# Kernel tuning notes

Measured on AMD Instinct MI355X. Metric: run time of the kernel, lower is better.

Reference implementation:

```python
import jax, jax.numpy as jnp
import numpy as np

HID_GNN = 64
HID_LSTM = 128
FUTURE = 24
N_HYDRO = 32
N_METEO = 64
B, T, E = 32, 168, 384
SLOPE = 0.01  # F.leaky_relu default


def setup_inputs() -> dict:
    key = jax.random.key(0)
    ks = jax.random.split(key, 12)
    N = N_HYDRO + N_METEO
    data_meteo = jax.random.normal(ks[0], (B, T, N_METEO, 1), jnp.float32)
    data_hydro = jax.random.normal(ks[1], (B, T, N_HYDRO, 1), jnp.float32)
    edge_index = jax.random.randint(ks[2], (2, E), 0, N, dtype=jnp.int64)
    # GraphConv(1, HID_GNN): out = lin_root(x) + lin_rel(sum_j x_j) + bias
    W_root = jax.random.normal(ks[3], (HID_GNN, 1), jnp.float32) * 1.0
    W_rel = jax.random.normal(ks[4], (HID_GNN, 1), jnp.float32) * 1.0
    b_gnn = jnp.zeros((HID_GNN,), jnp.float32)
    # Per-station LSTM weights (torch gate order i,f,g,o), stacked over stations
    sih = 1.0 / np.sqrt(HID_GNN)
    shh = 1.0 / np.sqrt(HID_LSTM)
    Wih = jax.random.normal(ks[5], (N_HYDRO, 4 * HID_LSTM, HID_GNN), jnp.float32) * sih
    Whh = jax.random.normal(ks[6], (N_HYDRO, 4 * HID_LSTM, HID_LSTM), jnp.float32) * shh
    bih = jnp.zeros((N_HYDRO, 4 * HID_LSTM), jnp.float32)
    bhh = jnp.zeros((N_HYDRO, 4 * HID_LSTM), jnp.float32)
    W_lin = jax.random.normal(ks[7], (FUTURE, HID_LSTM), jnp.float32) * shh
    b_lin = jnp.zeros((FUTURE,), jnp.float32)
    return {"data_meteo": data_meteo, "data_hydro": data_hydro, "edge_index": edge_index,
            "W_root": W_root, "W_rel": W_rel, "b_gnn": b_gnn,
            "Wih": Wih, "Whh": Whh, "bih": bih, "bhh": bhh,
            "W_lin": W_lin, "b_lin": b_lin}


def _lstm_last(xs, Wih_s, Whh_s, b_s):
    # xs: [B,T,D]; one station's LSTM; returns last hidden [B,H]
    H = Whh_s.shape[1]
    h0 = jnp.zeros((xs.shape[0], H), xs.dtype)

    def step(carry, xt):
        h, c = carry
        gates = xt @ Wih_s.T + h @ Whh_s.T + b_s  # [B,4H]
        i, f, g, o = jnp.split(gates, 4, axis=-1)
        c = jax.nn.sigmoid(f) * c + jax.nn.sigmoid(i) * jnp.tanh(g)
        h = jax.nn.sigmoid(o) * jnp.tanh(c)
        return (h, c), None

    (hT, _), _ = jax.lax.scan(step, (h0, h0), jnp.swapaxes(xs, 0, 1))
    return hT


def reference(data_meteo, data_hydro, edge_index, W_root, W_rel, b_gnn,
              Wih, Whh, bih, bhh, W_lin, b_lin):
    Bn, Tn, Nh, F = data_hydro.shape
    Nm = data_meteo.shape[2]
    N = Nh + Nm
    # [B,T,N,1] -> one graph per (b,t); same edge_index in every graph
    x = jnp.concatenate([data_hydro, data_meteo], axis=2).reshape(Bn * Tn, N, F)
    src, dst = edge_index[0], edge_index[1]
    agg = jnp.zeros_like(x).at[:, dst].add(x[:, src])  # sum aggregation
    h = x @ W_root.T + agg @ W_rel.T + b_gnn          # GraphConv, [G,N,HID_GNN]
    h = jax.nn.leaky_relu(h, SLOPE)
    hydro = h.reshape(Bn, Tn, N, -1)[:, :, :Nh, :]    # [B,T,Nh,HID_GNN]
    # per-station LSTM: vmap over station axis with station-specific weights
    last = jax.vmap(_lstm_last, in_axes=(2, 0, 0, 0))(hydro, Wih, Whh, bih + bhh)  # [Nh,B,H]
    pred = last @ W_lin.T + b_lin                     # [Nh,B,FUTURE]
    pred = jnp.swapaxes(pred, 0, 1)                   # [B,Nh,FUTURE]
    return jax.nn.leaky_relu(pred, SLOPE)
```

## Files before the change

kernel.cpp:

```cpp
#include <hip/hip_runtime.h>

typedef unsigned short u16;
typedef unsigned int u32;
typedef __attribute__((ext_vector_type(8))) short short8;
typedef __attribute__((ext_vector_type(4))) float floatx4;
typedef __attribute__((ext_vector_type(4))) float float4v;

#define B_ 32
#define T_ 168
#define NH_ 32
#define NM_ 64
#define E_ 384
#define HL_ 128
#define FUT_ 24
#define SLOPE_ 0.01f
#define XP_ 80
#define HP_ 144
#define WIH_LP 72
#define WHH_LP 136
#define OVL_E (T_ * 4 * XP_)

static __device__ __forceinline__ float b2f(u16 u) {
  u32 v = ((u32)u) << 16;
  return __builtin_bit_cast(float, v);
}
static __device__ __forceinline__ u16 f2bf(float f) {
  u32 x = __builtin_bit_cast(u32, f);
  u32 r = (x + 0x7fffu + ((x >> 16) & 1u)) >> 16;
  return (u16)r;
}
static __device__ __forceinline__ float fexp2(float x) { return __builtin_amdgcn_exp2f(x); }
static __device__ __forceinline__ float frcp(float x) { return __builtin_amdgcn_rcpf(x); }
static __device__ __forceinline__ float sigm(float x) {
  return frcp(1.0f + fexp2(-1.4426950408889634f * x));
}
static __device__ __forceinline__ float tanh_fast(float x) {
  return 1.0f - 2.0f * frcp(1.0f + fexp2(2.8853900817779268f * x));
}
static __device__ __forceinline__ float sel4(floatx4 v, int r) {
  float m0 = (r & 1) ? v[1] : v[0];
  float m1 = (r & 1) ? v[3] : v[2];
  return (r & 2) ? m1 : m0;
}
static __device__ __forceinline__ float lrelu(float x) { return fmaxf(x, SLOPE_ * x); }

__launch_bounds__(512, 2)
__global__ void fused_kernel(const float* __restrict__ dm, const float* __restrict__ dh,
                             const int* __restrict__ eidx,
                             const float* __restrict__ Wroot, const float* __restrict__ Wrel,
                             const float* __restrict__ bgnn,
                             const float* __restrict__ Wih, const float* __restrict__ Whh,
                             const float* __restrict__ bih, const float* __restrict__ bhh,
                             const float* __restrict__ Wlin, const float* __restrict__ blin,
                             float* __restrict__ out) {
  const int s = blockIdx.x & 31;
  const int bg = blockIdx.x >> 5;
  const int tid = threadIdx.x;
  const int w = tid >> 6;
  const int lane = tid & 63;
  const int cm = lane & 15;
  const int q = lane >> 4;
  const int b = cm & 3;
  const int rho = cm >> 2;

  __shared__ __align__(16) u16 ovl[OVL_E];
  __shared__ __align__(16) u16 hbuf[2 * 4 * HP_];
  __shared__ float xh_lds[4][T_];
  __shared__ float ag_lds[4][T_];
  __shared__ float wr_s[64], wv_s[64], bg_s[64];
  __shared__ int srcs[E_];
  __shared__ int nsrc, iflag;

  if (tid == 0) { nsrc = 0; iflag = 0; }
  for (int i = tid; i < 2 * 4 * HP_; i += 512) hbuf[i] = 0;
  __syncthreads();

  {
    int odd = 0;
    for (int e = tid; e < E_; e += 512) odd |= eidx[2 * e + 1];
    if (odd) atomicOr(&iflag, 1);
  }
  __syncthreads();
  const bool i32 = iflag != 0;

  for (int e = tid; e < E_; e += 512) {
    int se = i32 ? eidx[e] : eidx[2 * e];
    int de = i32 ? eidx[E_ + e] : eidx[2 * E_ + 2 * e];
    if (de == s) { int i = atomicAdd(&nsrc, 1); srcs[i] = se; }
  }
  if (tid < 64) { wr_s[tid] = Wroot[tid]; wv_s[tid] = Wrel[tid]; bg_s[tid] = bgnn[tid]; }
  for (int i = tid; i < 4 * T_; i += 512) {
    int bb = i / T_, t = i % T_;
    xh_lds[bb][t] = dh[((size_t)(bg * 4 + bb) * T_ + t) * NH_ + s];
  }
  floatx4 bias_init[4];
#pragma unroll
  for (int blk = 0; blk < 4; blk++)
#pragma unroll
    for (int r = 0; r < 4; r++) {
      const int nb = blk * 128 + w * 16 + q * 4 + r;
      bias_init[blk][r] = bih[s * 512 + nb] + bhh[s * 512 + nb];
    }
  __syncthreads();

  const int ns = nsrc;
  for (int i = tid; i < 4 * T_; i += 512) {
    int bb = i / T_, t = i % T_;
    size_t gb = (size_t)(bg * 4 + bb) * T_ + t;
    float a = 0.f;
    for (int j = 0; j < ns; j++) {
      int sr = srcs[j];
      a += (sr < NH_) ? dh[gb * NH_ + sr] : dm[gb * NM_ + (sr - NH_)];
    }
    ag_lds[bb][t] = a;
  }

  short8 Af[4][6];
  const int nl = w * 16 + cm;
  __syncthreads();
  {
    const float* g = Wih + (size_t)s * 512 * 64;
#pragma unroll
    for (int it = 0; it < 16; it++) {
      int j = tid + it * 512;
      float4v v = *(const float4v*)(g + 4 * j);
      u16* dst = ovl + (j >> 4) * WIH_LP + (j & 15) * 4;
      dst[0] = f2bf(v[0]); dst[1] = f2bf(v[1]); dst[2] = f2bf(v[2]); dst[3] = f2bf(v[3]);
    }
  }
  __syncthreads();
#pragma unroll
  for (int blk = 0; blk < 4; blk++)
#pragma unroll
    for (int kk = 0; kk < 2; kk++)
      Af[blk][kk] = *(const short8*)(ovl + (blk * 128 + nl) * WIH_LP + kk * 32 + q * 8);
  __syncthreads();
  {
    const float* g = Whh + (size_t)s * 512 * 128;
#pragma unroll
    for (int it = 0; it < 16; it++) {
      int j = tid + it * 512;
      float4v v = *(const float4v*)(g + 4 * j);
      u16* dst = ovl + (j >> 5) * WHH_LP + (j & 31) * 4;
      dst[0] = f2bf(v[0]); dst[1] = f2bf(v[1]); dst[2] = f2bf(v[2]); dst[3] = f2bf(v[3]);
    }
  }
  __syncthreads();
#pragma unroll
  for (int blk = 0; blk < 2; blk++)
#pragma unroll
    for (int kk = 0; kk < 4; kk++)
      Af[blk][2 + kk] = *(const short8*)(ovl + (blk * 128 + nl) * WHH_LP + kk * 32 + q * 8);
  __syncthreads();
  {
    const float* g = Whh + ((size_t)s * 512 + 256) * 128;
#pragma unroll
    for (int it = 0; it < 16; it++) {
      int j = tid + it * 512;
      float4v v = *(const float4v*)(g + 4 * j);
      u16* dst = ovl + (j >> 5) * WHH_LP + (j & 31) * 4;
      dst[0] = f2bf(v[0]); dst[1] = f2bf(v[1]); dst[2] = f2bf(v[2]); dst[3] = f2bf(v[3]);
    }
  }
  __syncthreads();
#pragma unroll
  for (int blk = 2; blk < 4; blk++)
#pragma unroll
    for (int kk = 0; kk < 4; kk++)
      Af[blk][2 + kk] = *(const short8*)(ovl + ((blk - 2) * 128 + nl) * WHH_LP + kk * 32 + q * 8);
  __syncthreads();

  {
    const int k = tid & 63;
    const int bb = (tid >> 6) & 3;
    const int th = tid >> 8;
    const float wrk = wr_s[k], wvk = wv_s[k], bgk = bg_s[k];
    for (int i = 0; i < T_ / 2; i++) {
      const int t = th * (T_ / 2) + i;
      const float xv = xh_lds[bb][t] * wrk + ag_lds[bb][t] * wvk + bgk;
      ovl[t * (4 * XP_) + bb * XP_ + k] = f2bf(lrelu(xv));
    }
  }
  __syncthreads();

  floatx4 accN[4];
  {
    short8 Bx0 = *(const short8*)(ovl + b * XP_ + q * 8);
    short8 Bx1 = *(const short8*)(ovl + b * XP_ + 32 + q * 8);
#pragma unroll
    for (int blk = 0; blk < 4; blk++) {
      accN[blk] = __builtin_amdgcn_mfma_f32_16x16x32_bf16(Af[blk][0], Bx0, bias_init[blk], 0, 0, 0);
      accN[blk] = __builtin_amdgcn_mfma_f32_16x16x32_bf16(Af[blk][1], Bx1, accN[blk], 0, 0, 0);
    }
  }
  float c = 0.0f;
#pragma unroll 2
  for (int t = 0; t < T_; t++) {
    const int p = t & 1, pn = p ^ 1;
    short8 Bh[4];
#pragma unroll
    for (int kk = 0; kk < 4; kk++)
      Bh[kk] = *(const short8*)(hbuf + p * (4 * HP_) + b * HP_ + kk * 32 + q * 8);

    floatx4 acc[4];
#pragma unroll
    for (int blk = 0; blk < 4; blk++) acc[blk] = accN[blk];
#pragma unroll
    for (int kk = 0; kk < 4; kk++)
#pragma unroll
      for (int blk = 0; blk < 4; blk++)
        acc[blk] = __builtin_amdgcn_mfma_f32_16x16x32_bf16(Af[blk][2 + kk], Bh[kk], acc[blk], 0, 0, 0);

    const float gi = sel4(acc[0], rho);
    const float gf = sel4(acc[1], rho);
    const float gg = sel4(acc[2], rho);
    const float go = sel4(acc[3], rho);
    c = sigm(gf) * c + sigm(gi) * tanh_fast(gg);
    const float hh = sigm(go) * tanh_fast(c);
    hbuf[pn * (4 * HP_) + b * HP_ + w * 16 + q * 4 + rho] = f2bf(hh);

    if (t + 1 < T_) {
      short8 Bx0 = *(const short8*)(ovl + (t + 1) * (4 * XP_) + b * XP_ + q * 8);
      short8 Bx1 = *(const short8*)(ovl + (t + 1) * (4 * XP_) + b * XP_ + 32 + q * 8);
#pragma unroll
      for (int blk = 0; blk < 4; blk++) {
        accN[blk] = __builtin_amdgcn_mfma_f32_16x16x32_bf16(Af[blk][0], Bx0, bias_init[blk], 0, 0, 0);
        accN[blk] = __builtin_amdgcn_mfma_f32_16x16x32_bf16(Af[blk][1], Bx1, accN[blk], 0, 0, 0);
      }
    }
    __syncthreads();
  }

  if (tid < 4 * FUT_) {
    const int bb = tid / FUT_;
    const int f = tid % FUT_;
    float a = blin[f];
#pragma unroll 8
    for (int k = 0; k < HL_; k++) a += b2f(hbuf[bb * HP_ + k]) * Wlin[f * HL_ + k];
    out[((size_t)(bg * 4 + bb) * NH_ + s) * FUT_ + f] = lrelu(a);
  }
}

extern "C" void kernel_launch(void* const* d_in, const int* in_sizes, int n_in,
                              void* d_out, int out_size, void* d_ws, size_t ws_size,
                              hipStream_t stream) {
  const float* dm = (const float*)d_in[0];
  const float* dh = (const float*)d_in[1];
  const int* eidx = (const int*)d_in[2];
  const float* Wroot = (const float*)d_in[3];
  const float* Wrel = (const float*)d_in[4];
  const float* bgnn = (const float*)d_in[5];
  const float* Wih = (const float*)d_in[6];
  const float* Whh = (const float*)d_in[7];
  const float* bih = (const float*)d_in[8];
  const float* bhh = (const float*)d_in[9];
  const float* Wlin = (const float*)d_in[10];
  const float* blin = (const float*)d_in[11];
  float* out = (float*)d_out;

  fused_kernel<<<256, 512, 0, stream>>>(dm, dh, eidx, Wroot, Wrel, bgnn, Wih, Whh,
                                        bih, bhh, Wlin, blin, out);
}
```

Baseline: 193.8 us.

## Fold activation exp2 scaling into weights and reorder gate MFMAs for overlap

Pre-scales the LSTM input, recurrent weights and biases by -log2(e), or 2*log2(e) for the g gate, so the per-step sigmoid and tanh need no multiply before exp2. Splits the recurrent MFMAs into two gate pairs so the exp2 of the g and i gates can start while the f and o MFMAs and the next step's input MFMAs are still issuing. Uses the hardware v_cvt_pk_bf16_f32 instruction for the bf16 store. Rounding the scaled weights to bf16 changes precision slightly.

```diff
diff --git a/kernel.cpp b/kernel.cpp
--- a/kernel.cpp
+++ b/kernel.cpp
@@ -20,6 +20,9 @@
 #define WHH_LP 136
 #define OVL_E (T_ * 4 * XP_)
 
+#define NS1_ (-1.4426950408889634f)
+#define S2_ (2.8853900817779268f)
+
 static __device__ __forceinline__ float b2f(u16 u) {
   u32 v = ((u32)u) << 16;
   return __builtin_bit_cast(float, v);
@@ -31,12 +34,6 @@
 }
 static __device__ __forceinline__ float fexp2(float x) { return __builtin_amdgcn_exp2f(x); }
 static __device__ __forceinline__ float frcp(float x) { return __builtin_amdgcn_rcpf(x); }
-static __device__ __forceinline__ float sigm(float x) {
-  return frcp(1.0f + fexp2(-1.4426950408889634f * x));
-}
-static __device__ __forceinline__ float tanh_fast(float x) {
-  return 1.0f - 2.0f * frcp(1.0f + fexp2(2.8853900817779268f * x));
-}
 static __device__ __forceinline__ float sel4(floatx4 v, int r) {
   float m0 = (r & 1) ? v[1] : v[0];
   float m1 = (r & 1) ? v[3] : v[2];
@@ -95,12 +92,14 @@
   }
   floatx4 bias_init[4];
 #pragma unroll
-  for (int blk = 0; blk < 4; blk++)
+  for (int blk = 0; blk < 4; blk++) {
+    const float scb = (blk == 2) ? S2_ : NS1_;
 #pragma unroll
     for (int r = 0; r < 4; r++) {
       const int nb = blk * 128 + w * 16 + q * 4 + r;
-      bias_init[blk][r] = bih[s * 512 + nb] + bhh[s * 512 + nb];
-    }
+      bias_init[blk][r] = (bih[s * 512 + nb] + bhh[s * 512 + nb]) * scb;
+    }
+  }
   __syncthreads();
 
   const int ns = nsrc;
@@ -124,8 +123,10 @@
     for (int it = 0; it < 16; it++) {
       int j = tid + it * 512;
       float4v v = *(const float4v*)(g + 4 * j);
+      const float sc = ((j >> 11) == 2) ? S2_ : NS1_;
       u16* dst = ovl + (j >> 4) * WIH_LP + (j & 15) * 4;
-      dst[0] = f2bf(v[0]); dst[1] = f2bf(v[1]); dst[2] = f2bf(v[2]); dst[3] = f2bf(v[3]);
+      dst[0] = f2bf(v[0] * sc); dst[1] = f2bf(v[1] * sc);
+      dst[2] = f2bf(v[2] * sc); dst[3] = f2bf(v[3] * sc);
     }
   }
   __syncthreads();
@@ -142,7 +143,8 @@
       int j = tid + it * 512;
       float4v v = *(const float4v*)(g + 4 * j);
       u16* dst = ovl + (j >> 5) * WHH_LP + (j & 31) * 4;
-      dst[0] = f2bf(v[0]); dst[1] = f2bf(v[1]); dst[2] = f2bf(v[2]); dst[3] = f2bf(v[3]);
+      dst[0] = f2bf(v[0] * NS1_); dst[1] = f2bf(v[1] * NS1_);
+      dst[2] = f2bf(v[2] * NS1_); dst[3] = f2bf(v[3] * NS1_);
     }
   }
   __syncthreads();
@@ -158,8 +160,10 @@
     for (int it = 0; it < 16; it++) {
       int j = tid + it * 512;
       float4v v = *(const float4v*)(g + 4 * j);
+      const float sc = (j < 4096) ? S2_ : NS1_;
       u16* dst = ovl + (j >> 5) * WHH_LP + (j & 31) * 4;
-      dst[0] = f2bf(v[0]); dst[1] = f2bf(v[1]); dst[2] = f2bf(v[2]); dst[3] = f2bf(v[3]);
+      dst[0] = f2bf(v[0] * sc); dst[1] = f2bf(v[1] * sc);
+      dst[2] = f2bf(v[2] * sc); dst[3] = f2bf(v[3] * sc);
     }
   }
   __syncthreads();
@@ -201,33 +205,50 @@
 #pragma unroll
     for (int kk = 0; kk < 4; kk++)
       Bh[kk] = *(const short8*)(hbuf + p * (4 * HP_) + b * HP_ + kk * 32 + q * 8);
-
-    floatx4 acc[4];
-#pragma unroll
-    for (int blk = 0; blk < 4; blk++) acc[blk] = accN[blk];
-#pragma unroll
-    for (int kk = 0; kk < 4; kk++)
-#pragma unroll
-      for (int blk = 0; blk < 4; blk++)
-        acc[blk] = __builtin_amdgcn_mfma_f32_16x16x32_bf16(Af[blk][2 + kk], Bh[kk], acc[blk], 0, 0, 0);
-
-    const float gi = sel4(acc[0], rho);
-    const float gf = sel4(acc[1], rho);
-    const float gg = sel4(acc[2], rho);
-    const float go = sel4(acc[3], rho);
-    c = sigm(gf) * c + sigm(gi) * tanh_fast(gg);
-    const float hh = sigm(go) * tanh_fast(c);
-    hbuf[pn * (4 * HP_) + b * HP_ + w * 16 + q * 4 + rho] = f2bf(hh);
-
-    if (t + 1 < T_) {
-      short8 Bx0 = *(const short8*)(ovl + (t + 1) * (4 * XP_) + b * XP_ + q * 8);
-      short8 Bx1 = *(const short8*)(ovl + (t + 1) * (4 * XP_) + b * XP_ + 32 + q * 8);
+    short8 Bx0n, Bx1n;
+    const bool more = (t + 1 < T_);
+    if (more) {
+      Bx0n = *(const short8*)(ovl + (t + 1) * (4 * XP_) + b * XP_ + q * 8);
+      Bx1n = *(const short8*)(ovl + (t + 1) * (4 * XP_) + b * XP_ + 32 + q * 8);
+    }
+
+    floatx4 a2 = accN[2], a0 = accN[0];
+#pragma unroll
+    for (int kk = 0; kk < 4; kk++) {
+      a2 = __builtin_amdgcn_mfma_f32_16x16x32_bf16(Af[2][2 + kk], Bh[kk], a2, 0, 0, 0);
+      a0 = __builtin_amdgcn_mfma_f32_16x16x32_bf16(Af[0][2 + kk], Bh[kk], a0, 0, 0, 0);
+    }
+    const float gg = sel4(a2, rho);
+    const float gi = sel4(a0, rho);
+    const float Eg = fexp2(gg);
+    const float Ei = fexp2(gi);
+
+    floatx4 a1 = accN[1], a3 = accN[3];
+#pragma unroll
+    for (int kk = 0; kk < 4; kk++) {
+      a1 = __builtin_amdgcn_mfma_f32_16x16x32_bf16(Af[1][2 + kk], Bh[kk], a1, 0, 0, 0);
+      a3 = __builtin_amdgcn_mfma_f32_16x16x32_bf16(Af[3][2 + kk], Bh[kk], a3, 0, 0, 0);
+    }
+    if (more) {
 #pragma unroll
       for (int blk = 0; blk < 4; blk++) {
-        accN[blk] = __builtin_amdgcn_mfma_f32_16x16x32_bf16(Af[blk][0], Bx0, bias_init[blk], 0, 0, 0);
-        accN[blk] = __builtin_amdgcn_mfma_f32_16x16x32_bf16(Af[blk][1], Bx1, accN[blk], 0, 0, 0);
+        accN[blk] = __builtin_amdgcn_mfma_f32_16x16x32_bf16(Af[blk][0], Bx0n, bias_init[blk], 0, 0, 0);
+        accN[blk] = __builtin_amdgcn_mfma_f32_16x16x32_bf16(Af[blk][1], Bx1n, accN[blk], 0, 0, 0);
       }
     }
+
+    const float tg = 1.0f - 2.0f * frcp(1.0f + Eg);
+    const float si = frcp(1.0f + Ei);
+    const float gf = sel4(a1, rho);
+    const float go = sel4(a3, rho);
+    const float sf = frcp(1.0f + fexp2(gf));
+    c = sf * c + si * tg;
+    const float tc = 1.0f - 2.0f * frcp(1.0f + fexp2(S2_ * c));
+    const float so = frcp(1.0f + fexp2(go));
+    const float hh = so * tc;
+    u32 pk;
+    asm("v_cvt_pk_bf16_f32 %0, %1, %2" : "=v"(pk) : "v"(hh), "v"(hh));
+    hbuf[pn * (4 * HP_) + b * HP_ + w * 16 + q * 4 + rho] = (u16)pk;
     __syncthreads();
   }
 
```

New measurement: 191.7 us. About the same (-1.1%).
